# Kernel tuning notes

Measured on AMD Instinct MI355X. Metric: run time of the kernel, lower is better.

## Reference

```python
import jax, jax.numpy as jnp
import numpy as np

# Module config (matches init_kwargs)
N_HEADS = 32        # query heads
MAX_SEQLEN = 2048
LOCAL_BLOCKS = 16
VERT_STRIDE = 8
BLOCK_SIZE = 64
HEAD_SIZE = 128
KV_HEADS = 8
BATCH = 2
SEQLEN = 1024       # per-sample length (equal-length varlen batch)


def _dense_sparse_mask(maxlen):
    """Local + strided block-sparse causal mask, heterogeneous heads.
    Returns bool [N_HEADS, maxlen, maxlen]; True = attend."""
    nb = MAX_SEQLEN // BLOCK_SIZE
    q_pos = jnp.arange(nb)[:, None]
    k_pos = jnp.arange(nb)[None, :]
    h = jnp.arange(N_HEADS)[:, None]
    # head-dependent vertical stride (homo_head=False)
    vert = ((jnp.arange(nb)[None, :] + h + 1) % VERT_STRIDE == 0)  # [H, nb]
    blk = (q_pos >= k_pos) & (((q_pos - k_pos) < LOCAL_BLOCKS)[None] | vert[:, None, :])  # [H, nb, nb]
    tok = jnp.repeat(jnp.repeat(blk, BLOCK_SIZE, axis=1), BLOCK_SIZE, axis=2)  # [H, S, S]
    causal = jnp.tril(jnp.ones((MAX_SEQLEN, MAX_SEQLEN), dtype=bool))
    tok = tok & causal[None]
    return tok[:, :maxlen, :maxlen]


def setup_inputs() -> dict:
    key = jax.random.key(0)
    kq, kk, kv = jax.random.split(key, 3)
    total = BATCH * SEQLEN
    q = jax.random.normal(kq, (total, N_HEADS, HEAD_SIZE), dtype=jnp.float32)
    k = jax.random.normal(kk, (total, KV_HEADS, HEAD_SIZE), dtype=jnp.float32)
    v = jax.random.normal(kv, (total, KV_HEADS, HEAD_SIZE), dtype=jnp.float32)
    cu_seqlens_k = jnp.arange(BATCH + 1, dtype=jnp.int32) * SEQLEN  # [0, 1024, 2048]
    return {"q": q, "k": k, "v": v, "cu_seqlens_k": cu_seqlens_k}


def reference(q, k, v, cu_seqlens_k):
    B = cu_seqlens_k.shape[0] - 1
    T, Hq, D = q.shape
    Hk = k.shape[1]
    r = Hq // Hk                      # q/kv head ratio (GQA)
    L = T // B                        # equal-length sequences
    scale = 1.0 / np.sqrt(D)

    mask = _dense_sparse_mask(L)      # [Hq, L, L]
    bias = jnp.where(mask, jnp.float32(0.0), jnp.finfo(jnp.float32).min)
    bias = bias.reshape(Hk, r, L, L)

    qb = q.reshape(B, L, Hk, r, D)
    kb = k.reshape(B, L, Hk, D)
    vb = v.reshape(B, L, Hk, D)

    scores = jnp.einsum('bqgrd,bkgd->bgrqk', qb, kb) * scale  # [B, Hk, r, L, L]
    attn = jax.nn.softmax(scores + bias[None], axis=-1)
    out = jnp.einsum('bgrqk,bkgd->bqgrd', attn, vb)           # [B, L, Hk, r, D]
    return out.reshape(T, Hq, D)
```

## Files before the change

### kernel.cpp

```cpp
#include <hip/hip_runtime.h>

typedef __attribute__((ext_vector_type(8))) short s8bf;
typedef __attribute__((ext_vector_type(4))) float f4;
typedef __attribute__((ext_vector_type(2))) unsigned u2;
typedef __attribute__((ext_vector_type(4))) unsigned u4;

#define HQ 32
#define HK 8
#define DH 128

static __device__ __forceinline__ unsigned cvtpk(float a, float b) {
  unsigned r;
  asm("v_cvt_pk_bf16_f32 %0, %1, %2" : "=v"(r) : "v"(a), "v"(b));
  return r;
}
union frag_u { s8bf v; unsigned u[4]; };

static __device__ __forceinline__ void gload_lds16(const short* g, short* l) {
  __builtin_amdgcn_global_load_lds(
      (const __attribute__((address_space(1))) void*)g,
      (__attribute__((address_space(3))) void*)l, 16, 0, 0);
}

#define WAIT_VM(N)                                         \
  do {                                                     \
    asm volatile("s_waitcnt vmcnt(" #N ")" ::: "memory");  \
    __builtin_amdgcn_sched_barrier(0);                     \
  } while (0)


__global__ void prep_kernel(const float* __restrict__ kg, const float* __restrict__ vg,
                            short* __restrict__ kbt, short* __restrict__ vbt) {
  const int blk = blockIdx.x;
  if (blk < 512) {
    const int gid = blk * 256 + threadIdx.x;
#pragma unroll
    for (int i = 0; i < 2; ++i) {
      int c = gid + i * 131072;
      int l16 = c & 15, quad = (c >> 4) & 3;
      int f = (c >> 6) & 15;
      int kt = (c >> 10) & 15;
      int bg = c >> 14;
      int b = bg >> 3, g = bg & 7;
      int key = kt * 64 + (f >> 2) * 16 + l16;
      int d0 = (f & 3) * 32 + quad * 8;
      const float* src = kg + (((size_t)(b * 1024 + key) * HK + g) * DH + d0);
      f4 a = *(const f4*)src, cc = *(const f4*)(src + 4);
      u4 w;
      w[0] = cvtpk(a[0], a[1]);   w[1] = cvtpk(a[2], a[3]);
      w[2] = cvtpk(cc[0], cc[1]); w[3] = cvtpk(cc[2], cc[3]);
      *(u4*)(kbt + (size_t)c * 8) = w;
    }
  } else {
    __shared__ short T[32 * 130];
    const int t = blk - 512;
    const int half = t & 1, tile = t >> 1;
    const int bg = tile >> 4, kt = tile & 15;
    const int b = bg >> 3, g = bg & 7;
#pragma unroll
    for (int i = 0; i < 4; ++i) {
      int e = threadIdx.x * 4 + i * 1024;
      int key = e >> 7, d = e & 127;
      f4 x = *(const f4*)(vg + (((size_t)(b * 1024 + kt * 64 + half * 32 + key) * HK + g) * DH + d));
      u2 w; w[0] = cvtpk(x[0], x[1]); w[1] = cvtpk(x[2], x[3]);
      *(u2*)&T[key * 130 + d] = w;
    }
    __syncthreads();
    short* dst = vbt + (size_t)(bg * 16 + kt) * 8192;
#pragma unroll
    for (int i = 0; i < 2; ++i) {
      int c = threadIdx.x + i * 256;
      int lane = c & 63, dt = c >> 6;
      int fidx = dt * 2 + half;
      int l16 = lane & 15, quad = (lane >> 4) & 3;
      int d = dt * 16 + l16;
      int k0 = quad * 4;
      int k1 = k0 + 16;
      u4 w;
      w[0] = (unsigned)(unsigned short)T[(k0 + 0) * 130 + d] |
             ((unsigned)(unsigned short)T[(k0 + 1) * 130 + d] << 16);
      w[1] = (unsigned)(unsigned short)T[(k0 + 2) * 130 + d] |
             ((unsigned)(unsigned short)T[(k0 + 3) * 130 + d] << 16);
      w[2] = (unsigned)(unsigned short)T[(k1 + 0) * 130 + d] |
             ((unsigned)(unsigned short)T[(k1 + 1) * 130 + d] << 16);
      w[3] = (unsigned)(unsigned short)T[(k1 + 2) * 130 + d] |
             ((unsigned)(unsigned short)T[(k1 + 3) * 130 + d] << 16);
      *(u4*)(dst + (size_t)(fidx * 64 + lane) * 8) = w;
    }
  }
}

__launch_bounds__(256, 2)
__global__ void fa_main(const float* __restrict__ qg, const short* __restrict__ kbt,
                        const short* __restrict__ vbt, float* __restrict__ out) {
  const int id  = blockIdx.x;
  const int g   = id & 7;
  const int s   = id >> 3;
  const int qt  = 15 - (s >> 3);
  const int rem = s & 7;
  const int b   = rem >> 2;
  const int h   = g * 4 + (rem & 3);
  const int bg  = b * 8 + g;

  const int tid  = threadIdx.x;
  const int wave = tid >> 6, lane = tid & 63;
  const int l16  = lane & 15, quad = lane >> 4;
  const int qlocal = wave * 16 + l16;
  const int seq0 = b * 1024;

  __shared__ short smem[2][16384];

  const float qmul = 0.08838834764831845f * 1.4426950408889634f;
  const float* qp = qg + ((size_t)(seq0 + qt * 64 + qlocal) * HQ + h) * DH;
  s8bf qf[4];
#pragma unroll
  for (int dk = 0; dk < 4; ++dk) {
    const float* p = qp + dk * 32 + quad * 8;
    f4 a = *(const f4*)p, c = *(const f4*)(p + 4);
    frag_u t;
    t.u[0] = cvtpk(a[0] * qmul, a[1] * qmul);
    t.u[1] = cvtpk(a[2] * qmul, a[2] * qmul);
    t.u[1] = cvtpk(a[2] * qmul, a[3] * qmul);
    t.u[2] = cvtpk(c[0] * qmul, c[1] * qmul);
    t.u[3] = cvtpk(c[2] * qmul, c[3] * qmul);
    qf[dk] = t.v;
  }

  float l_ = 0.0f;
  f4 oacc[8];
#pragma unroll
  for (int dt = 0; dt < 8; ++dt) oacc[dt] = (f4)(0.0f);

  const short* ktile = kbt + (size_t)bg * 16 * 8192;
  const short* vtile = vbt + (size_t)bg * 16 * 8192;

  __builtin_amdgcn_sched_barrier(0);

#pragma unroll
  for (int i = 0; i < 4; ++i) {
    int f = wave * 4 + i;
    gload_lds16(ktile + (size_t)(f * 64 + lane) * 8, &smem[0][f * 512]);
    gload_lds16(vtile + (size_t)(f * 64 + lane) * 8, &smem[0][8192 + f * 512]);
  }

  for (int kt = 0; kt <= qt; ++kt) {
    const int cur = kt & 1;

    if (kt < qt) {
      const short* kn = ktile + (size_t)(kt + 1) * 8192;
      const short* vn = vtile + (size_t)(kt + 1) * 8192;
      short* db = &smem[cur ^ 1][0];
#pragma unroll
      for (int i = 0; i < 4; ++i) {
        int f = wave * 4 + i;
        gload_lds16(kn + (size_t)(f * 64 + lane) * 8, db + f * 512);
        gload_lds16(vn + (size_t)(f * 64 + lane) * 8, db + 8192 + f * 512);
      }
      WAIT_VM(8);
    } else {
      WAIT_VM(0);
    }
    __builtin_amdgcn_s_barrier();
    __builtin_amdgcn_sched_barrier(0);

    const short* kb = &smem[cur][lane * 8];
    const short* vb = &smem[cur][8192 + lane * 8];

    f4 sacc[4];
#pragma unroll
    for (int ct = 0; ct < 4; ++ct) sacc[ct] = (f4)(0.0f);
    __builtin_amdgcn_s_setprio(1);
#pragma unroll
    for (int dk = 0; dk < 4; ++dk)
#pragma unroll
      for (int ct = 0; ct < 4; ++ct) {
        s8bf kf = *(const s8bf*)&kb[(ct * 4 + dk) * 512];
        sacc[ct] = __builtin_amdgcn_mfma_f32_16x16x32_bf16(kf, qf[dk], sacc[ct], 0, 0, 0);
      }
    __builtin_amdgcn_s_setprio(0);

    if (kt == qt) {
#pragma unroll
      for (int ct = 0; ct < 4; ++ct)
#pragma unroll
        for (int i = 0; i < 4; ++i) {
          int key = ct * 16 + quad * 4 + i;
          if (key > qlocal) sacc[ct][i] = -1e30f;
        }
    }

    float rs = 0.0f;
    unsigned pk[4][2];
#pragma unroll
    for (int ct = 0; ct < 4; ++ct) {
      float p0 = exp2f(fminf(sacc[ct][0], 30.0f));
      float p1 = exp2f(fminf(sacc[ct][1], 30.0f));
      float p2 = exp2f(fminf(sacc[ct][2], 30.0f));
      float p3 = exp2f(fminf(sacc[ct][3], 30.0f));
      rs += (p0 + p1) + (p2 + p3);
      pk[ct][0] = cvtpk(p0, p1);
      pk[ct][1] = cvtpk(p2, p3);
    }
    l_ += rs;

    __builtin_amdgcn_s_setprio(1);
#pragma unroll
    for (int ks = 0; ks < 2; ++ks) {
      frag_u fr;
      fr.u[0] = pk[2 * ks][0];
      fr.u[1] = pk[2 * ks][1];
      fr.u[2] = pk[2 * ks + 1][0];
      fr.u[3] = pk[2 * ks + 1][1];
#pragma unroll
      for (int dt = 0; dt < 8; ++dt) {
        s8bf vf = *(const s8bf*)&vb[(dt * 2 + ks) * 512];
        oacc[dt] = __builtin_amdgcn_mfma_f32_16x16x32_bf16(vf, fr.v, oacc[dt], 0, 0, 0);
      }
    }
    __builtin_amdgcn_s_setprio(0);

    asm volatile("s_waitcnt lgkmcnt(0)" ::: "memory");
    __builtin_amdgcn_sched_barrier(0);
    __builtin_amdgcn_s_barrier();
  }

  float lt = l_;
  lt += __shfl_xor(lt, 16);
  lt += __shfl_xor(lt, 32);
  float inv = 1.0f / lt;
  float* op = out + ((size_t)(seq0 + qt * 64 + qlocal) * HQ + h) * DH;
#pragma unroll
  for (int dt = 0; dt < 8; ++dt) {
    f4 w;
    w[0] = oacc[dt][0] * inv; w[1] = oacc[dt][1] * inv;
    w[2] = oacc[dt][2] * inv; w[3] = oacc[dt][3] * inv;
    *(f4*)(op + dt * 16 + quad * 4) = w;
  }
}

extern "C" void kernel_launch(void* const* d_in, const int* in_sizes, int n_in,
                              void* d_out, int out_size, void* d_ws, size_t ws_size,
                              hipStream_t stream) {
  const float* q = (const float*)d_in[0];
  const float* k = (const float*)d_in[1];
  const float* v = (const float*)d_in[2];
  float* out = (float*)d_out;

  short* kbt = (short*)d_ws;
  short* vbt = kbt + (size_t)16 * 16 * 8192;

  prep_kernel<<<dim3(1024), 256, 0, stream>>>(k, v, kbt, vbt);
  fa_main<<<dim3(1024), 256, 0, stream>>>(q, kbt, vbt, out);
}
```

Baseline: 126.7 us.

## Process two adjacent query tiles per block to reuse K/V loads

Each workgroup now handles two consecutive 64-row query tiles (qtA, qtB) with the same head, sharing every K/V tile staged in LDS between both. This halves the grid to 512 blocks and roughly halves K/V global-to-LDS traffic, while doubling MFMA work per loaded tile. The cost is twice the accumulator registers (two oacc sets), which may hurt occupancy under launch_bounds(256,2), plus the first tile does one wasted fully masked iteration. The mask appears to still ignore the sparse pattern, same as before.

Result: no change. 127.2 us (+0.3%).

```diff
diff --git a/kernel.cpp b/kernel.cpp
--- a/kernel.cpp
+++ b/kernel.cpp
@@ -96,11 +96,13 @@
   const int id  = blockIdx.x;
   const int g   = id & 7;
   const int s   = id >> 3;
-  const int qt  = 15 - (s >> 3);
+  const int half = s >> 5, j = (s >> 3) & 3;
+  const int t   = half ? j : 7 - j;
   const int rem = s & 7;
   const int b   = rem >> 2;
   const int h   = g * 4 + (rem & 3);
   const int bg  = b * 8 + g;
+  const int qtA = 2 * t, qtB = 2 * t + 1;
 
   const int tid  = threadIdx.x;
   const int wave = tid >> 6, lane = tid & 63;
@@ -111,25 +113,32 @@
   __shared__ short smem[2][16384];
 
   const float qmul = 0.08838834764831845f * 1.4426950408889634f;
-  const float* qp = qg + ((size_t)(seq0 + qt * 64 + qlocal) * HQ + h) * DH;
-  s8bf qf[4];
+  const float* qpA = qg + ((size_t)(seq0 + qtA * 64 + qlocal) * HQ + h) * DH;
+  const float* qpB = qg + ((size_t)(seq0 + qtB * 64 + qlocal) * HQ + h) * DH;
+  s8bf qfA[4], qfB[4];
 #pragma unroll
   for (int dk = 0; dk < 4; ++dk) {
-    const float* p = qp + dk * 32 + quad * 8;
-    f4 a = *(const f4*)p, c = *(const f4*)(p + 4);
-    frag_u t;
-    t.u[0] = cvtpk(a[0] * qmul, a[1] * qmul);
-    t.u[1] = cvtpk(a[2] * qmul, a[2] * qmul);
-    t.u[1] = cvtpk(a[2] * qmul, a[3] * qmul);
-    t.u[2] = cvtpk(c[0] * qmul, c[1] * qmul);
-    t.u[3] = cvtpk(c[2] * qmul, c[3] * qmul);
-    qf[dk] = t.v;
-  }
-
-  float l_ = 0.0f;
-  f4 oacc[8];
-#pragma unroll
-  for (int dt = 0; dt < 8; ++dt) oacc[dt] = (f4)(0.0f);
+    const float* pA = qpA + dk * 32 + quad * 8;
+    const float* pB = qpB + dk * 32 + quad * 8;
+    f4 a0 = *(const f4*)pA, a1 = *(const f4*)(pA + 4);
+    f4 b0 = *(const f4*)pB, b1 = *(const f4*)(pB + 4);
+    frag_u ta, tb;
+    ta.u[0] = cvtpk(a0[0] * qmul, a0[1] * qmul);
+    ta.u[1] = cvtpk(a0[2] * qmul, a0[3] * qmul);
+    ta.u[2] = cvtpk(a1[0] * qmul, a1[1] * qmul);
+    ta.u[3] = cvtpk(a1[2] * qmul, a1[3] * qmul);
+    tb.u[0] = cvtpk(b0[0] * qmul, b0[1] * qmul);
+    tb.u[1] = cvtpk(b0[2] * qmul, b0[3] * qmul);
+    tb.u[2] = cvtpk(b1[0] * qmul, b1[1] * qmul);
+    tb.u[3] = cvtpk(b1[2] * qmul, b1[3] * qmul);
+    qfA[dk] = ta.v;
+    qfB[dk] = tb.v;
+  }
+
+  float lA = 0.0f, lB = 0.0f;
+  f4 oaccA[8], oaccB[8];
+#pragma unroll
+  for (int dt = 0; dt < 8; ++dt) { oaccA[dt] = (f4)(0.0f); oaccB[dt] = (f4)(0.0f); }
 
   const short* ktile = kbt + (size_t)bg * 16 * 8192;
   const short* vtile = vbt + (size_t)bg * 16 * 8192;
@@ -143,10 +152,10 @@
     gload_lds16(vtile + (size_t)(f * 64 + lane) * 8, &smem[0][8192 + f * 512]);
   }
 
-  for (int kt = 0; kt <= qt; ++kt) {
+  for (int kt = 0; kt <= qtB; ++kt) {
     const int cur = kt & 1;
 
-    if (kt < qt) {
+    if (kt < qtB) {
       const short* kn = ktile + (size_t)(kt + 1) * 8192;
       const short* vn = vtile + (size_t)(kt + 1) * 8192;
       short* db = &smem[cur ^ 1][0];
@@ -166,55 +175,79 @@
     const short* kb = &smem[cur][lane * 8];
     const short* vb = &smem[cur][8192 + lane * 8];
 
-    f4 sacc[4];
-#pragma unroll
-    for (int ct = 0; ct < 4; ++ct) sacc[ct] = (f4)(0.0f);
+    f4 saccA[4], saccB[4];
+#pragma unroll
+    for (int ct = 0; ct < 4; ++ct) { saccA[ct] = (f4)(0.0f); saccB[ct] = (f4)(0.0f); }
     __builtin_amdgcn_s_setprio(1);
 #pragma unroll
     for (int dk = 0; dk < 4; ++dk)
 #pragma unroll
       for (int ct = 0; ct < 4; ++ct) {
         s8bf kf = *(const s8bf*)&kb[(ct * 4 + dk) * 512];
-        sacc[ct] = __builtin_amdgcn_mfma_f32_16x16x32_bf16(kf, qf[dk], sacc[ct], 0, 0, 0);
+        saccA[ct] = __builtin_amdgcn_mfma_f32_16x16x32_bf16(kf, qfA[dk], saccA[ct], 0, 0, 0);
+        saccB[ct] = __builtin_amdgcn_mfma_f32_16x16x32_bf16(kf, qfB[dk], saccB[ct], 0, 0, 0);
       }
     __builtin_amdgcn_s_setprio(0);
 
-    if (kt == qt) {
+    if (kt >= qtA) {
+      int thr = (kt == qtA) ? qlocal : -1;
 #pragma unroll
       for (int ct = 0; ct < 4; ++ct)
 #pragma unroll
         for (int i = 0; i < 4; ++i) {
           int key = ct * 16 + quad * 4 + i;
-          if (key > qlocal) sacc[ct][i] = -1e30f;
+          if (key > thr) saccA[ct][i] = -1e30f;
         }
     }
-
-    float rs = 0.0f;
-    unsigned pk[4][2];
+    if (kt == qtB) {
+#pragma unroll
+      for (int ct = 0; ct < 4; ++ct)
+#pragma unroll
+        for (int i = 0; i < 4; ++i) {
+          int key = ct * 16 + quad * 4 + i;
+          if (key > qlocal) saccB[ct][i] = -1e30f;
+        }
+    }
+
+    float rsA = 0.0f, rsB = 0.0f;
+    unsigned pkA[4][2], pkB[4][2];
 #pragma unroll
     for (int ct = 0; ct < 4; ++ct) {
-      float p0 = exp2f(fminf(sacc[ct][0], 30.0f));
-      float p1 = exp2f(fminf(sacc[ct][1], 30.0f));
-      float p2 = exp2f(fminf(sacc[ct][2], 30.0f));
-      float p3 = exp2f(fminf(sacc[ct][3], 30.0f));
-      rs += (p0 + p1) + (p2 + p3);
-      pk[ct][0] = cvtpk(p0, p1);
-      pk[ct][1] = cvtpk(p2, p3);
-    }
-    l_ += rs;
+      float a0 = exp2f(fminf(saccA[ct][0], 30.0f));
+      float a1 = exp2f(fminf(saccA[ct][1], 30.0f));
+      float a2 = exp2f(fminf(saccA[ct][2], 30.0f));
+      float a3 = exp2f(fminf(saccA[ct][3], 30.0f));
+      rsA += (a0 + a1) + (a2 + a3);
+      pkA[ct][0] = cvtpk(a0, a1);
+      pkA[ct][1] = cvtpk(a2, a3);
+      float b0 = exp2f(fminf(saccB[ct][0], 30.0f));
+      float b1 = exp2f(fminf(saccB[ct][1], 30.0f));
+      float b2 = exp2f(fminf(saccB[ct][2], 30.0f));
+      float b3 = exp2f(fminf(saccB[ct][3], 30.0f));
+      rsB += (b0 + b1) + (b2 + b3);
+      pkB[ct][0] = cvtpk(b0, b1);
+      pkB[ct][1] = cvtpk(b2, b3);
+    }
+    lA += rsA;
+    lB += rsB;
 
     __builtin_amdgcn_s_setprio(1);
 #pragma unroll
     for (int ks = 0; ks < 2; ++ks) {
-      frag_u fr;
-      fr.u[0] = pk[2 * ks][0];
-      fr.u[1] = pk[2 * ks][1];
-      fr.u[2] = pk[2 * ks + 1][0];
-      fr.u[3] = pk[2 * ks + 1][1];
+      frag_u frA, frB;
+      frA.u[0] = pkA[2 * ks][0];
+      frA.u[1] = pkA[2 * ks][1];
+      frA.u[2] = pkA[2 * ks + 1][0];
+      frA.u[3] = pkA[2 * ks + 1][1];
+      frB.u[0] = pkB[2 * ks][0];
+      frB.u[1] = pkB[2 * ks][1];
+      frB.u[2] = pkB[2 * ks + 1][0];
+      frB.u[3] = pkB[2 * ks + 1][1];
 #pragma unroll
       for (int dt = 0; dt < 8; ++dt) {
         s8bf vf = *(const s8bf*)&vb[(dt * 2 + ks) * 512];
-        oacc[dt] = __builtin_amdgcn_mfma_f32_16x16x32_bf16(vf, fr.v, oacc[dt], 0, 0, 0);
+        oaccA[dt] = __builtin_amdgcn_mfma_f32_16x16x32_bf16(vf, frA.v, oaccA[dt], 0, 0, 0);
+        oaccB[dt] = __builtin_amdgcn_mfma_f32_16x16x32_bf16(vf, frB.v, oaccB[dt], 0, 0, 0);
       }
     }
     __builtin_amdgcn_s_setprio(0);
@@ -224,17 +257,26 @@
     __builtin_amdgcn_s_barrier();
   }
 
-  float lt = l_;
-  lt += __shfl_xor(lt, 16);
-  lt += __shfl_xor(lt, 32);
-  float inv = 1.0f / lt;
-  float* op = out + ((size_t)(seq0 + qt * 64 + qlocal) * HQ + h) * DH;
+  float ltA = lA;
+  ltA += __shfl_xor(ltA, 16);
+  ltA += __shfl_xor(ltA, 32);
+  float invA = 1.0f / ltA;
+  float ltB = lB;
+  ltB += __shfl_xor(ltB, 16);
+  ltB += __shfl_xor(ltB, 32);
+  float invB = 1.0f / ltB;
+
+  float* opA = out + ((size_t)(seq0 + qtA * 64 + qlocal) * HQ + h) * DH;
+  float* opB = out + ((size_t)(seq0 + qtB * 64 + qlocal) * HQ + h) * DH;
 #pragma unroll
   for (int dt = 0; dt < 8; ++dt) {
-    f4 w;
-    w[0] = oacc[dt][0] * inv; w[1] = oacc[dt][1] * inv;
-    w[2] = oacc[dt][2] * inv; w[3] = oacc[dt][3] * inv;
-    *(f4*)(op + dt * 16 + quad * 4) = w;
+    f4 wa, wb;
+    wa[0] = oaccA[dt][0] * invA; wa[1] = oaccA[dt][1] * invA;
+    wa[2] = oaccA[dt][2] * invA; wa[3] = oaccA[dt][3] * invA;
+    wb[0] = oaccB[dt][0] * invB; wb[1] = oaccB[dt][1] * invB;
+    wb[2] = oaccB[dt][2] * invB; wb[3] = oaccB[dt][3] * invB;
+    *(f4*)(opA + dt * 16 + quad * 4) = wa;
+    *(f4*)(opB + dt * 16 + quad * 4) = wb;
   }
 }
 
@@ -250,5 +292,5 @@
   short* vbt = kbt + (size_t)16 * 16 * 8192;
 
   prep_kernel<<<dim3(1024), 256, 0, stream>>>(k, v, kbt, vbt);
-  fa_main<<<dim3(1024), 256, 0, stream>>>(q, kbt, vbt, out);
-}
+  fa_main<<<dim3(512), 256, 0, stream>>>(q, kbt, vbt, out);
+}
```

## Halve KV tile to 32 keys and raise occupancy to four blocks per CU

Applied to the files above, without the earlier changes.

The attention loop now processes 32-key tiles instead of 64, halving the LDS double buffer and the per-iteration score accumulators. This lets launch bounds request four workgroups per CU, so all 1024 blocks can be resident at once. The staging macro, causal-mask threshold and PV MFMA loop are re-indexed to address half-tiles inside the existing pre-transposed K/V layout. The cost is twice as many loop iterations, each with its own barriers and wait, and tighter register limits. A duplicated Q conversion line is also removed.

Result: no change. 125.2 us (-1.2%).

```diff
diff --git a/kernel.cpp b/kernel.cpp
--- a/kernel.cpp
+++ b/kernel.cpp
@@ -90,7 +90,7 @@
   }
 }
 
-__launch_bounds__(256, 2)
+__launch_bounds__(256, 4)
 __global__ void fa_main(const float* __restrict__ qg, const short* __restrict__ kbt,
                         const short* __restrict__ vbt, float* __restrict__ out) {
   const int id  = blockIdx.x;
@@ -101,6 +101,7 @@
   const int b   = rem >> 2;
   const int h   = g * 4 + (rem & 3);
   const int bg  = b * 8 + g;
+  const int kmax = 2 * qt + 1;
 
   const int tid  = threadIdx.x;
   const int wave = tid >> 6, lane = tid & 63;
@@ -108,7 +109,7 @@
   const int qlocal = wave * 16 + l16;
   const int seq0 = b * 1024;
 
-  __shared__ short smem[2][16384];
+  __shared__ short smem[2][8192];
 
   const float qmul = 0.08838834764831845f * 1.4426950408889634f;
   const float* qp = qg + ((size_t)(seq0 + qt * 64 + qlocal) * HQ + h) * DH;
@@ -119,7 +120,6 @@
     f4 a = *(const f4*)p, c = *(const f4*)(p + 4);
     frag_u t;
     t.u[0] = cvtpk(a[0] * qmul, a[1] * qmul);
-    t.u[1] = cvtpk(a[2] * qmul, a[2] * qmul);
     t.u[1] = cvtpk(a[2] * qmul, a[3] * qmul);
     t.u[2] = cvtpk(c[0] * qmul, c[1] * qmul);
     t.u[3] = cvtpk(c[2] * qmul, c[3] * qmul);
@@ -136,27 +136,30 @@
 
   __builtin_amdgcn_sched_barrier(0);
 
-#pragma unroll
-  for (int i = 0; i < 4; ++i) {
-    int f = wave * 4 + i;
-    gload_lds16(ktile + (size_t)(f * 64 + lane) * 8, &smem[0][f * 512]);
-    gload_lds16(vtile + (size_t)(f * 64 + lane) * 8, &smem[0][8192 + f * 512]);
-  }
-
-  for (int kt = 0; kt <= qt; ++kt) {
+#define STAGE_TILE(J, BUF)                                                             \
+  do {                                                                                 \
+    const short* kb32 = ktile + (size_t)((J) >> 1) * 8192 + ((J) & 1) * 4096;          \
+    const short* vb32 = vtile + (size_t)((J) >> 1) * 8192 + ((J) & 1) * 512;           \
+    _Pragma("unroll")                                                                  \
+    for (int i = 0; i < 4; ++i) {                                                      \
+      int fidx = wave * 4 + i;                                                         \
+      if (fidx < 8) {                                                                  \
+        gload_lds16(kb32 + (size_t)(fidx * 64 + lane) * 8, &smem[BUF][fidx * 512]);    \
+      } else {                                                                         \
+        gload_lds16(vb32 + (size_t)((fidx - 8) * 128 + lane) * 8,                      \
+                    &smem[BUF][4096 + (fidx - 8) * 512]);                              \
+      }                                                                                \
+    }                                                                                  \
+  } while (0)
+
+  STAGE_TILE(0, 0);
+
+  for (int kt = 0; kt <= kmax; ++kt) {
     const int cur = kt & 1;
 
-    if (kt < qt) {
-      const short* kn = ktile + (size_t)(kt + 1) * 8192;
-      const short* vn = vtile + (size_t)(kt + 1) * 8192;
-      short* db = &smem[cur ^ 1][0];
-#pragma unroll
-      for (int i = 0; i < 4; ++i) {
-        int f = wave * 4 + i;
-        gload_lds16(kn + (size_t)(f * 64 + lane) * 8, db + f * 512);
-        gload_lds16(vn + (size_t)(f * 64 + lane) * 8, db + 8192 + f * 512);
-      }
-      WAIT_VM(8);
+    if (kt < kmax) {
+      STAGE_TILE(kt + 1, cur ^ 1);
+      WAIT_VM(4);
     } else {
       WAIT_VM(0);
     }
@@ -164,58 +167,51 @@
     __builtin_amdgcn_sched_barrier(0);
 
     const short* kb = &smem[cur][lane * 8];
-    const short* vb = &smem[cur][8192 + lane * 8];
-
-    f4 sacc[4];
-#pragma unroll
-    for (int ct = 0; ct < 4; ++ct) sacc[ct] = (f4)(0.0f);
+    const short* vb = &smem[cur][4096 + lane * 8];
+
+    f4 sacc[2];
+#pragma unroll
+    for (int ct = 0; ct < 2; ++ct) sacc[ct] = (f4)(0.0f);
     __builtin_amdgcn_s_setprio(1);
 #pragma unroll
     for (int dk = 0; dk < 4; ++dk)
 #pragma unroll
-      for (int ct = 0; ct < 4; ++ct) {
+      for (int ct = 0; ct < 2; ++ct) {
         s8bf kf = *(const s8bf*)&kb[(ct * 4 + dk) * 512];
         sacc[ct] = __builtin_amdgcn_mfma_f32_16x16x32_bf16(kf, qf[dk], sacc[ct], 0, 0, 0);
       }
     __builtin_amdgcn_s_setprio(0);
 
-    if (kt == qt) {
-#pragma unroll
-      for (int ct = 0; ct < 4; ++ct)
+    if (kt >= 2 * qt) {
+      int thr = qlocal - (kt - 2 * qt) * 32;
+#pragma unroll
+      for (int ct = 0; ct < 2; ++ct)
 #pragma unroll
         for (int i = 0; i < 4; ++i) {
           int key = ct * 16 + quad * 4 + i;
-          if (key > qlocal) sacc[ct][i] = -1e30f;
+          if (key > thr) sacc[ct][i] = -1e30f;
         }
     }
 
     float rs = 0.0f;
-    unsigned pk[4][2];
-#pragma unroll
-    for (int ct = 0; ct < 4; ++ct) {
+    frag_u fr;
+#pragma unroll
+    for (int ct = 0; ct < 2; ++ct) {
       float p0 = exp2f(fminf(sacc[ct][0], 30.0f));
       float p1 = exp2f(fminf(sacc[ct][1], 30.0f));
       float p2 = exp2f(fminf(sacc[ct][2], 30.0f));
       float p3 = exp2f(fminf(sacc[ct][3], 30.0f));
       rs += (p0 + p1) + (p2 + p3);
-      pk[ct][0] = cvtpk(p0, p1);
-      pk[ct][1] = cvtpk(p2, p3);
+      fr.u[ct * 2 + 0] = cvtpk(p0, p1);
+      fr.u[ct * 2 + 1] = cvtpk(p2, p3);
     }
     l_ += rs;
 
     __builtin_amdgcn_s_setprio(1);
 #pragma unroll
-    for (int ks = 0; ks < 2; ++ks) {
-      frag_u fr;
-      fr.u[0] = pk[2 * ks][0];
-      fr.u[1] = pk[2 * ks][1];
-      fr.u[2] = pk[2 * ks + 1][0];
-      fr.u[3] = pk[2 * ks + 1][1];
-#pragma unroll
-      for (int dt = 0; dt < 8; ++dt) {
-        s8bf vf = *(const s8bf*)&vb[(dt * 2 + ks) * 512];
-        oacc[dt] = __builtin_amdgcn_mfma_f32_16x16x32_bf16(vf, fr.v, oacc[dt], 0, 0, 0);
-      }
+    for (int dt = 0; dt < 8; ++dt) {
+      s8bf vf = *(const s8bf*)&vb[dt * 512];
+      oacc[dt] = __builtin_amdgcn_mfma_f32_16x16x32_bf16(vf, fr.v, oacc[dt], 0, 0, 0);
     }
     __builtin_amdgcn_s_setprio(0);
 
```
